# Kernel tuning notes

Measured on AMD Instinct MI355X. Metric: run time of the kernel, lower is better.

The kernel has to match this reference:

```python
import jax, jax.numpy as jnp
import numpy as np

N, K, D = 65536, 1024, 256


def setup_inputs() -> dict:
    key = jax.random.key(0)
    k1, k2 = jax.random.split(key)
    e = jax.random.normal(k1, (N, D), dtype=jnp.float32)
    # module inits codebook uniform in [-1/K, 1/K]
    weight = jax.random.uniform(k2, (K, D), dtype=jnp.float32,
                                minval=-1.0 / K, maxval=1.0 / K)
    return {"e": e, "weight": weight}


def reference(e, weight):
    distances = (jnp.sum(e * e, axis=1, keepdims=True)
                 - 2.0 * jnp.matmul(e, weight.T)
                 + jnp.sum(weight * weight, axis=1))
    encoding_indices = jnp.argmin(distances, axis=1)            # [N]
    # one-hot @ weight is just a gather
    quantized = weight[encoding_indices]                        # [N, D]
    commitment_loss = jnp.mean((jax.lax.stop_gradient(quantized) - e) ** 2)
    counts = jnp.zeros((K,), dtype=jnp.float32).at[encoding_indices].add(1.0)
    codebook_usage = counts.max() / counts.sum()
    # straight-through estimator
    quantized = e + jax.lax.stop_gradient(quantized - e)
    return quantized, encoding_indices, commitment_loss, codebook_usage
```

## Files before the change

### kernel.cpp

```cpp
#include <hip/hip_runtime.h>

typedef __attribute__((ext_vector_type(8))) short short8;
typedef __attribute__((ext_vector_type(4))) float floatx4;

#define N_ROWS 65536
#define K_CB   1024
#define D_DIM  256

#define TAU 4.0e-4f
#define BLINE 520

#define OFF_WN     262144
#define OFF_FIXCNT 266240
#define OFF_HIST   266496
#define OFF_IDX    270592
#define OFF_LIST   532736
#define OFF_PART   794880
#define OFF_WFRAG  827392
#define OFF_KEYS   1351680
#define OFF_WT     1875968

__device__ __forceinline__ float pw128_sq(const float4* p) {
#pragma clang fp contract(off)
    float4 q0 = p[0], q1 = p[1];
    float r0 = q0.x * q0.x, r1 = q0.y * q0.y, r2 = q0.z * q0.z, r3 = q0.w * q0.w;
    float r4 = q1.x * q1.x, r5 = q1.y * q1.y, r6 = q1.z * q1.z, r7 = q1.w * q1.w;
    for (int i = 1; i < 16; ++i) {
        float4 u0 = p[2 * i], u1 = p[2 * i + 1];
        r0 = r0 + u0.x * u0.x; r1 = r1 + u0.y * u0.y;
        r2 = r2 + u0.z * u0.z; r3 = r3 + u0.w * u0.w;
        r4 = r4 + u1.x * u1.x; r5 = r5 + u1.y * u1.y;
        r6 = r6 + u1.z * u1.z; r7 = r7 + u1.w * u1.w;
    }
    return ((r0 + r1) + (r2 + r3)) + ((r4 + r5) + (r6 + r7));
}
__device__ __forceinline__ float pw128_sq_lds(const double* p) {
#pragma clang fp contract(off)
    float r[8];
    #pragma unroll
    for (int j = 0; j < 8; ++j) { float x = (float)p[j]; r[j] = x * x; }
    for (int i = 1; i < 16; ++i) {
        #pragma unroll
        for (int j = 0; j < 8; ++j) { float x = (float)p[8 * i + j]; r[j] = r[j] + x * x; }
    }
    return ((r[0] + r[1]) + (r[2] + r[3])) + ((r[4] + r[5]) + (r[6] + r[7]));
}
__device__ __forceinline__ float rownorm_np(const float* row) {
#pragma clang fp contract(off)
    float s0 = pw128_sq((const float4*)row);
    float s1 = pw128_sq((const float4*)(row + 128));
    return s0 + s1;
}
__device__ __forceinline__ float np_dist(float A, float m, float Ck) {
#pragma clang fp contract(off)
    float Bv = 2.0f * m;
    float t  = A - Bv;
    return t + Ck;
}
__device__ __forceinline__ unsigned short bf16_rne(float x) {
    unsigned u = __float_as_uint(x);
    unsigned r = u + 0x7fff + ((u >> 16) & 1);
    return (unsigned short)(r >> 16);
}

#define PRS 260
__global__ __launch_bounds__(256) void k_prep(
        const float* __restrict__ wg,
        float* __restrict__ wn,
        unsigned short* __restrict__ wfrag, float* __restrict__ wt) {
    __shared__ __align__(16) float es[32 * PRS];
    const int tid = threadIdx.x;
    const int bx  = blockIdx.x;
    if (bx < 4) {
        int row = bx * 256 + tid;
        wn[row] = rownorm_np(wg + (size_t)row * D_DIM);
    } else if (bx < 132) {
        int t = (bx - 4) * 256 + tid;
        int col = t >> 5, kc = t & 31;
        const float4* src = (const float4*)(wg + (size_t)col * D_DIM + kc * 8);
        float4 v0 = src[0], v1 = src[1];
        const float a[8] = {v0.x, v0.y, v0.z, v0.w, v1.x, v1.y, v1.z, v1.w};
        short8 h;
        #pragma unroll
        for (int i = 0; i < 8; ++i) h[i] = (short)bf16_rne(a[i]);
        *(short8*)(wfrag + ((size_t)kc * 1024 + col) * 8) = h;
    } else {
        float (*tw)[PRS] = (float(*)[PRS])es;
        const int cb = bx - 132;
        const int c0 = cb * 32;
        #pragma unroll
        for (int it = 0; it < 8; ++it) {
            int idx = it * 256 + tid;
            int code = idx >> 6, f4 = idx & 63;
            *(float4*)&tw[code][f4 * 4] =
                *(const float4*)(wg + (size_t)(c0 + code) * D_DIM + f4 * 4);
        }
        __syncthreads();
        const int j = tid & 31, dg = tid >> 5;
        #pragma unroll
        for (int dd = 0; dd < 32; ++dd) {
            int d = dd * 8 + dg;
            wt[(size_t)d * K_CB + c0 + j] = tw[j][d];
        }
    }
}

__global__ __launch_bounds__(256, 2) void k_dist(
        const float* __restrict__ eg, const unsigned short* __restrict__ wfrag,
        const float* __restrict__ wn,
        int* __restrict__ idx_ws, int* __restrict__ fixlist, int* __restrict__ fixcnt) {
    __shared__ __align__(16) unsigned short Bs[32 * BLINE];
    __shared__ float wnS[K_CB];
    const int tid  = threadIdx.x;
    const int lane = tid & 63;
    const int wv   = tid >> 6;
    const int q    = lane >> 4;
    const int m15  = lane & 15;
    const int waveRow = blockIdx.x * 128 + wv * 32;

    #pragma unroll
    for (int i = 0; i < 4; ++i) wnS[tid + i * 256] = wn[tid + i * 256];

    short8 afh0[8], afh1[8];
    #pragma unroll
    for (int mt = 0; mt < 2; ++mt) {
        const float* rowp = eg + (size_t)(waveRow + mt * 16 + m15) * D_DIM + q * 8;
        #pragma unroll
        for (int win = 0; win < 8; ++win) {
            const float4* pa = (const float4*)(rowp + win * 32);
            float4 x0 = pa[0], x1 = pa[1];
            const float a[8] = {x0.x, x0.y, x0.z, x0.w, x1.x, x1.y, x1.z, x1.w};
            short8 h;
            #pragma unroll
            for (int i = 0; i < 8; ++i) h[i] = (short)bf16_rne(a[i]);
            if (mt == 0) afh0[win] = h; else afh1[win] = h;
        }
    }

    float best[8], sec[8];
    int bidx[8];
    #pragma unroll
    for (int s = 0; s < 8; ++s) { best[s] = 3.4e38f; sec[s] = 3.4e38f; bidx[s] = 0; }

    for (int cb = 0; cb < 16; ++cb) {
        __syncthreads();
        #pragma unroll
        for (int t = 0; t < 8; ++t) {
            int L = wv * 8 + t;
            const unsigned short* src = wfrag + ((size_t)L * 1024 + cb * 64) * 8 + lane * 8;
            __builtin_amdgcn_global_load_lds(
                (const __attribute__((address_space(1))) unsigned int*)src,
                (__attribute__((address_space(3))) unsigned int*)&Bs[L * BLINE],
                16, 0, 0);
        }
        __syncthreads();

        #pragma unroll
        for (int nt = 0; nt < 4; ++nt) {
            floatx4 acc0 = (floatx4){0.f, 0.f, 0.f, 0.f};
            floatx4 acc1 = (floatx4){0.f, 0.f, 0.f, 0.f};
            #pragma unroll
            for (int win = 0; win < 8; ++win) {
                int kc = win * 4 + q;
                short8 bfh = *(short8*)&Bs[kc * BLINE + (nt * 16 + m15) * 8];
                acc0 = __builtin_amdgcn_mfma_f32_16x16x32_bf16(afh0[win], bfh, acc0, 0, 0, 0);
                acc1 = __builtin_amdgcn_mfma_f32_16x16x32_bf16(afh1[win], bfh, acc1, 0, 0, 0);
            }
            int col = cb * 64 + nt * 16 + m15;
            float Ck = wnS[col];
            #pragma unroll
            for (int reg = 0; reg < 4; ++reg) {
                float d0 = __builtin_fmaf(-2.0f, acc0[reg], Ck);
                bool lt0 = d0 < best[reg];
                sec[reg]  = __builtin_amdgcn_fmed3f(d0, best[reg], sec[reg]);
                best[reg] = fminf(d0, best[reg]);
                bidx[reg] = lt0 ? col : bidx[reg];
                float d1 = __builtin_fmaf(-2.0f, acc1[reg], Ck);
                int s1 = 4 + reg;
                bool lt1 = d1 < best[s1];
                sec[s1]  = __builtin_amdgcn_fmed3f(d1, best[s1], sec[s1]);
                best[s1] = fminf(d1, best[s1]);
                bidx[s1] = lt1 ? col : bidx[s1];
            }
        }
    }

    #pragma unroll
    for (int s = 0; s < 8; ++s) {
        float b = best[s], se = sec[s];
        int ix = bidx[s];
        #pragma unroll
        for (int m = 1; m < 16; m <<= 1) {
            float bo = __shfl_xor(b, m, 64);
            float so = __shfl_xor(se, m, 64);
            int   io = __shfl_xor(ix, m, 64);
            float ns = fminf(fminf(se, so), fmaxf(b, bo));
            if (bo < b || (bo == b && io < ix)) { b = bo; ix = io; }
            se = ns;
        }
        if (m15 == 0) {
            int row = waveRow + (s >> 2) * 16 + q * 4 + (s & 3);
            idx_ws[row] = ix;
            if (se - b < TAU) {
                int p = atomicAdd(fixcnt, 1);
                fixlist[p] = row;
            }
        }
    }
}

#define FG_ROWS 8
__global__ __launch_bounds__(256) void k_fixup(
        const float* __restrict__ eg, const float* __restrict__ wt,
        const float* __restrict__ wnorm,
        const int* __restrict__ fixlist, const int* __restrict__ fixcnt,
        unsigned long long* __restrict__ keys) {
    __shared__ double xs[FG_ROWS][D_DIM];
    __shared__ float AnS[FG_ROWS];
    const int tid = threadIdx.x;
    const int cnt = *fixcnt;
    if (cnt == 0) return;
    const int ngroups = (cnt + FG_ROWS - 1) / FG_ROWS;
    const int ntiles  = ngroups * 2;
    const int rowg = tid >> 7;
    const int cg   = tid & 127;
    for (int t = blockIdx.x; t < ntiles; t += gridDim.x) {
        const int g     = t >> 1;
        const int chunk = t & 1;
        __syncthreads();
        int rows[FG_ROWS];
        #pragma unroll
        for (int i = 0; i < FG_ROWS; ++i) {
            int j = g * FG_ROWS + i;
            rows[i] = fixlist[j < cnt ? j : cnt - 1];
        }
        #pragma unroll
        for (int i = 0; i < FG_ROWS; ++i)
            xs[i][tid] = (double)eg[(size_t)rows[i] * D_DIM + tid];
        __syncthreads();

        if (tid < 16) {
            int row = tid >> 1, half = tid & 1;
            float s = pw128_sq_lds(&xs[row][half * 128]);
            float so = __shfl_xor(s, 1, 64);
            if (half == 0) AnS[row] = s + so;
        }

        const int c0 = chunk * 512 + cg * 4;
        float Cw[4];
        #pragma unroll
        for (int c = 0; c < 4; ++c) Cw[c] = wnorm[c0 + c];

        double s[4][4];
        #pragma unroll
        for (int r = 0; r < 4; ++r)
            #pragma unroll
            for (int c = 0; c < 4; ++c) s[r][c] = 0.0;

        #pragma unroll 2
        for (int d = 0; d < D_DIM; d += 2) {
            float4 wa = *(const float4*)(wt + (size_t)d * K_CB + c0);
            float4 wb = *(const float4*)(wt + (size_t)(d + 1) * K_CB + c0);
            double wad[4] = {(double)wa.x, (double)wa.y, (double)wa.z, (double)wa.w};
            double wbd[4] = {(double)wb.x, (double)wb.y, (double)wb.z, (double)wb.w};
            #pragma unroll
            for (int r = 0; r < 4; ++r) {
                double2 e2 = *(const double2*)&xs[rowg * 4 + r][d];
                #pragma unroll
                for (int c = 0; c < 4; ++c)
                    s[r][c] += e2.x * wad[c] + e2.y * wbd[c];
            }
        }
        __syncthreads();

        #pragma unroll
        for (int r = 0; r < 4; ++r) {
            float An = AnS[rowg * 4 + r];
            unsigned long long key = 0xFFFFFFFFFFFFFFFFull;
            #pragma unroll
            for (int c = 0; c < 4; ++c) {
                float dq = np_dist(An, (float)s[r][c], Cw[c]);
                unsigned u = __float_as_uint(dq);
                unsigned key32 = u ^ (((unsigned)((int)u >> 31)) | 0x80000000u);
                unsigned long long kk =
                    ((unsigned long long)key32 << 32) | (unsigned)(c0 + c);
                key = kk < key ? kk : key;
            }
            #pragma unroll
            for (int m = 1; m < 64; m <<= 1) {
                unsigned long long o = __shfl_xor(key, m, 64);
                key = (o < key) ? o : key;
            }
            int j = g * FG_ROWS + rowg * 4 + r;
            if ((tid & 63) == 0 && j < cnt) atomicMin(&keys[j], key);
        }
    }
}

__global__ void k_fixscatter(const int* __restrict__ fixlist, const int* __restrict__ fixcnt,
                             const unsigned long long* __restrict__ keys,
                             int* __restrict__ idx_ws) {
    const int cnt = *fixcnt;
    for (int j = blockIdx.x * blockDim.x + threadIdx.x; j < cnt;
         j += gridDim.x * blockDim.x)
        idx_ws[fixlist[j]] = (int)(keys[j] & 0xFFFFFFFFull);
}

__global__ void k_final(const float* __restrict__ eg, const float* __restrict__ wg,
                        const int* __restrict__ idx_ws, float* __restrict__ qout,
                        float* __restrict__ iout, int* __restrict__ hist,
                        double* __restrict__ partials) {
    const int tid  = threadIdx.x;
    const int sub  = tid >> 6;
    const int lane = tid & 63;
    const int rowBase = blockIdx.x * 16;
    double acc = 0.0;
    #pragma unroll
    for (int g = 0; g < 4; ++g) {
        int row = rowBase + g * 4 + sub;
        int k = idx_ws[row];
        float4 ev = ((const float4*)(eg + (size_t)row * D_DIM))[lane];
        float4 wv = ((const float4*)(wg + (size_t)k   * D_DIM))[lane];
        float dx = wv.x - ev.x, dy = wv.y - ev.y, dz = wv.z - ev.z, dw = wv.w - ev.w;
        float4 qv = {ev.x + dx, ev.y + dy, ev.z + dz, ev.w + dw};
        ((float4*)(qout + (size_t)row * D_DIM))[lane] = qv;
        acc += (double)(dx * dx) + (double)(dy * dy)
             + (double)(dz * dz) + (double)(dw * dw);
        if (lane == 0) {
            iout[row] = (float)k;
            atomicAdd(&hist[k], 1);
        }
    }
    __shared__ double red[256];
    red[tid] = acc;
    __syncthreads();
    for (int st = 128; st > 0; st >>= 1) {
        if (tid < st) red[tid] += red[tid + st];
        __syncthreads();
    }
    if (tid == 0) partials[blockIdx.x] = red[0];
}

__global__ void k_scalars(const int* __restrict__ hist, const double* __restrict__ partials,
                          float* __restrict__ sout) {
    const int tid = threadIdx.x;
    double s = 0.0;
    for (int j = tid; j < N_ROWS / 16; j += 256) s += partials[j];
    int m = 0;
    for (int j = tid; j < K_CB; j += 256) m = max(m, hist[j]);
    __shared__ double rs[256];
    __shared__ int    rm[256];
    rs[tid] = s; rm[tid] = m;
    __syncthreads();
    for (int st = 128; st > 0; st >>= 1) {
        if (tid < st) { rs[tid] += rs[tid + st]; rm[tid] = max(rm[tid], rm[tid + st]); }
        __syncthreads();
    }
    if (tid == 0) {
        sout[0] = (float)(rs[0] / (double)((size_t)N_ROWS * D_DIM));
        sout[1] = (float)rm[0] / 65536.0f;
    }
}

extern "C" void kernel_launch(void* const* d_in, const int* in_sizes, int n_in,
                              void* d_out, int out_size, void* d_ws, size_t ws_size,
                              hipStream_t stream) {
    const float* e = (const float*)d_in[0];
    const float* w = (const float*)d_in[1];
    float* out  = (float*)d_out;
    float* qout = out;
    float* iout = out + (size_t)N_ROWS * D_DIM;
    float* sout = iout + N_ROWS;

    char* ws = (char*)d_ws;
    float*  wn       = (float*) (ws + OFF_WN);
    int*    fixcnt   = (int*)   (ws + OFF_FIXCNT);
    int*    hist     = (int*)   (ws + OFF_HIST);
    int*    idxp     = (int*)   (ws + OFF_IDX);
    int*    list     = (int*)   (ws + OFF_LIST);
    double* partials = (double*)(ws + OFF_PART);
    unsigned short* wfrag = (unsigned short*)(ws + OFF_WFRAG);
    unsigned long long* keys = (unsigned long long*)(ws + OFF_KEYS);
    float*  wt       = (float*) (ws + OFF_WT);

    hipMemsetAsync(ws + OFF_FIXCNT, 0, 4352, stream);
    hipMemsetAsync(ws + OFF_KEYS, 0xFF, 524288, stream);

    hipLaunchKernelGGL(k_prep,       dim3(164),         dim3(256), 0, stream, w, wn, wfrag, wt);
    hipLaunchKernelGGL(k_dist,       dim3(512),         dim3(256), 0, stream, e, wfrag, wn, idxp, list, fixcnt);
    hipLaunchKernelGGL(k_fixup,      dim3(2048),        dim3(256), 0, stream, e, wt, wn, list, fixcnt, keys);
    hipLaunchKernelGGL(k_fixscatter, dim3(64),          dim3(256), 0, stream, list, fixcnt, keys, idxp);
    hipLaunchKernelGGL(k_final,      dim3(N_ROWS / 16), dim3(256), 0, stream, e, w, idxp, qout, iout, hist, partials);
    hipLaunchKernelGGL(k_scalars,    dim3(1),           dim3(256), 0, stream, hist, partials, sout);
}
```

Before: 314.7 us.

## Double-buffer codebook tiles in k_dist and use fp32 top-2 rescoring in fixup

```diff
diff --git a/kernel.cpp b/kernel.cpp
--- a/kernel.cpp
+++ b/kernel.cpp
@@ -34,17 +34,6 @@
     }
     return ((r0 + r1) + (r2 + r3)) + ((r4 + r5) + (r6 + r7));
 }
-__device__ __forceinline__ float pw128_sq_lds(const double* p) {
-#pragma clang fp contract(off)
-    float r[8];
-    #pragma unroll
-    for (int j = 0; j < 8; ++j) { float x = (float)p[j]; r[j] = x * x; }
-    for (int i = 1; i < 16; ++i) {
-        #pragma unroll
-        for (int j = 0; j < 8; ++j) { float x = (float)p[8 * i + j]; r[j] = r[j] + x * x; }
-    }
-    return ((r[0] + r[1]) + (r[2] + r[3])) + ((r[4] + r[5]) + (r[6] + r[7]));
-}
 __device__ __forceinline__ float rownorm_np(const float* row) {
 #pragma clang fp contract(off)
     float s0 = pw128_sq((const float4*)row);
@@ -61,6 +50,11 @@
     unsigned u = __float_as_uint(x);
     unsigned r = u + 0x7fff + ((u >> 16) & 1);
     return (unsigned short)(r >> 16);
+}
+__device__ __forceinline__ unsigned long long dist_key(float d, int idx) {
+    unsigned u = __float_as_uint(d);
+    unsigned k32 = u ^ (((unsigned)((int)u >> 31)) | 0x80000000u);
+    return ((unsigned long long)k32 << 32) | (unsigned)idx;
 }
 
 #define PRS 260
@@ -109,7 +103,7 @@
         const float* __restrict__ eg, const unsigned short* __restrict__ wfrag,
         const float* __restrict__ wn,
         int* __restrict__ idx_ws, int* __restrict__ fixlist, int* __restrict__ fixcnt) {
-    __shared__ __align__(16) unsigned short Bs[32 * BLINE];
+    __shared__ __align__(16) unsigned short Bs[2][32 * BLINE];
     __shared__ float wnS[K_CB];
     const int tid  = threadIdx.x;
     const int lane = tid & 63;
@@ -142,19 +136,31 @@
     #pragma unroll
     for (int s = 0; s < 8; ++s) { best[s] = 3.4e38f; sec[s] = 3.4e38f; bidx[s] = 0; }
 
+    #pragma unroll
+    for (int t = 0; t < 8; ++t) {
+        int L = wv * 8 + t;
+        const unsigned short* src = wfrag + ((size_t)L * 1024) * 8 + lane * 8;
+        __builtin_amdgcn_global_load_lds(
+            (const __attribute__((address_space(1))) unsigned int*)src,
+            (__attribute__((address_space(3))) unsigned int*)&Bs[0][L * BLINE],
+            16, 0, 0);
+    }
+    __syncthreads();
+
     for (int cb = 0; cb < 16; ++cb) {
-        __syncthreads();
-        #pragma unroll
-        for (int t = 0; t < 8; ++t) {
-            int L = wv * 8 + t;
-            const unsigned short* src = wfrag + ((size_t)L * 1024 + cb * 64) * 8 + lane * 8;
-            __builtin_amdgcn_global_load_lds(
-                (const __attribute__((address_space(1))) unsigned int*)src,
-                (__attribute__((address_space(3))) unsigned int*)&Bs[L * BLINE],
-                16, 0, 0);
-        }
-        __syncthreads();
-
+        const int p = cb & 1;
+        if (cb < 15) {
+            #pragma unroll
+            for (int t = 0; t < 8; ++t) {
+                int L = wv * 8 + t;
+                const unsigned short* src =
+                    wfrag + ((size_t)L * 1024 + (cb + 1) * 64) * 8 + lane * 8;
+                __builtin_amdgcn_global_load_lds(
+                    (const __attribute__((address_space(1))) unsigned int*)src,
+                    (__attribute__((address_space(3))) unsigned int*)&Bs[p ^ 1][L * BLINE],
+                    16, 0, 0);
+            }
+        }
         #pragma unroll
         for (int nt = 0; nt < 4; ++nt) {
             floatx4 acc0 = (floatx4){0.f, 0.f, 0.f, 0.f};
@@ -162,7 +168,7 @@
             #pragma unroll
             for (int win = 0; win < 8; ++win) {
                 int kc = win * 4 + q;
-                short8 bfh = *(short8*)&Bs[kc * BLINE + (nt * 16 + m15) * 8];
+                short8 bfh = *(short8*)&Bs[p][kc * BLINE + (nt * 16 + m15) * 8];
                 acc0 = __builtin_amdgcn_mfma_f32_16x16x32_bf16(afh0[win], bfh, acc0, 0, 0, 0);
                 acc1 = __builtin_amdgcn_mfma_f32_16x16x32_bf16(afh1[win], bfh, acc1, 0, 0, 0);
             }
@@ -183,6 +189,7 @@
                 bidx[s1] = lt1 ? col : bidx[s1];
             }
         }
+        __syncthreads();
     }
 
     #pragma unroll
@@ -211,13 +218,14 @@
 
 #define FG_ROWS 8
 __global__ __launch_bounds__(256) void k_fixup(
-        const float* __restrict__ eg, const float* __restrict__ wt,
-        const float* __restrict__ wnorm,
+        const float* __restrict__ eg, const float* __restrict__ wg,
+        const float* __restrict__ wt, const float* __restrict__ wnorm,
         const int* __restrict__ fixlist, const int* __restrict__ fixcnt,
         unsigned long long* __restrict__ keys) {
-    __shared__ double xs[FG_ROWS][D_DIM];
+    __shared__ __align__(16) float xs[FG_ROWS][D_DIM];
     __shared__ float AnS[FG_ROWS];
-    const int tid = threadIdx.x;
+    const int tid  = threadIdx.x;
+    const int lane = tid & 63;
     const int cnt = *fixcnt;
     if (cnt == 0) return;
     const int ngroups = (cnt + FG_ROWS - 1) / FG_ROWS;
@@ -236,14 +244,14 @@
         }
         #pragma unroll
         for (int i = 0; i < FG_ROWS; ++i)
-            xs[i][tid] = (double)eg[(size_t)rows[i] * D_DIM + tid];
+            xs[i][tid] = eg[(size_t)rows[i] * D_DIM + tid];
         __syncthreads();
 
         if (tid < 16) {
             int row = tid >> 1, half = tid & 1;
-            float s = pw128_sq_lds(&xs[row][half * 128]);
-            float so = __shfl_xor(s, 1, 64);
-            if (half == 0) AnS[row] = s + so;
+            float sN = pw128_sq((const float4*)&xs[row][half * 128]);
+            float so = __shfl_xor(sN, 1, 64);
+            if (half == 0) AnS[row] = sN + so;
         }
 
         const int c0 = chunk * 512 + cg * 4;
@@ -251,48 +259,67 @@
         #pragma unroll
         for (int c = 0; c < 4; ++c) Cw[c] = wnorm[c0 + c];
 
-        double s[4][4];
+        float s[4][4];
         #pragma unroll
         for (int r = 0; r < 4; ++r)
             #pragma unroll
-            for (int c = 0; c < 4; ++c) s[r][c] = 0.0;
+            for (int c = 0; c < 4; ++c) s[r][c] = 0.f;
 
         #pragma unroll 2
         for (int d = 0; d < D_DIM; d += 2) {
             float4 wa = *(const float4*)(wt + (size_t)d * K_CB + c0);
             float4 wb = *(const float4*)(wt + (size_t)(d + 1) * K_CB + c0);
-            double wad[4] = {(double)wa.x, (double)wa.y, (double)wa.z, (double)wa.w};
-            double wbd[4] = {(double)wb.x, (double)wb.y, (double)wb.z, (double)wb.w};
             #pragma unroll
             for (int r = 0; r < 4; ++r) {
-                double2 e2 = *(const double2*)&xs[rowg * 4 + r][d];
-                #pragma unroll
-                for (int c = 0; c < 4; ++c)
-                    s[r][c] += e2.x * wad[c] + e2.y * wbd[c];
+                float2 e2 = *(const float2*)&xs[rowg * 4 + r][d];
+                s[r][0] += e2.x * wa.x + e2.y * wb.x;
+                s[r][1] += e2.x * wa.y + e2.y * wb.y;
+                s[r][2] += e2.x * wa.z + e2.y * wb.z;
+                s[r][3] += e2.x * wa.w + e2.y * wb.w;
             }
         }
         __syncthreads();
 
         #pragma unroll
         for (int r = 0; r < 4; ++r) {
-            float An = AnS[rowg * 4 + r];
-            unsigned long long key = 0xFFFFFFFFFFFFFFFFull;
+            const int R = rowg * 4 + r;
+            float An = AnS[R];
+            unsigned long long kb = 0xFFFFFFFFFFFFFFFFull, ks = 0xFFFFFFFFFFFFFFFFull;
             #pragma unroll
             for (int c = 0; c < 4; ++c) {
-                float dq = np_dist(An, (float)s[r][c], Cw[c]);
-                unsigned u = __float_as_uint(dq);
-                unsigned key32 = u ^ (((unsigned)((int)u >> 31)) | 0x80000000u);
-                unsigned long long kk =
-                    ((unsigned long long)key32 << 32) | (unsigned)(c0 + c);
-                key = kk < key ? kk : key;
+                float dq = np_dist(An, s[r][c], Cw[c]);
+                unsigned long long kk = dist_key(dq, c0 + c);
+                if (kk < kb) { ks = kb; kb = kk; }
+                else if (kk < ks) { ks = kk; }
             }
             #pragma unroll
             for (int m = 1; m < 64; m <<= 1) {
-                unsigned long long o = __shfl_xor(key, m, 64);
-                key = (o < key) ? o : key;
-            }
-            int j = g * FG_ROWS + rowg * 4 + r;
-            if ((tid & 63) == 0 && j < cnt) atomicMin(&keys[j], key);
+                unsigned long long ko = __shfl_xor(kb, m, 64);
+                unsigned long long so = __shfl_xor(ks, m, 64);
+                if (ko < kb) { ks = (so < kb) ? so : kb; kb = ko; }
+                else         { ks = (ko < ks) ? ko : ks; }
+            }
+            int cand = (int)((lane < 32 ? kb : ks) & 0xFFFFFFFFull);
+            const float* wrow = wg + (size_t)cand * D_DIM + (lane & 31) * 8;
+            const float* erow = &xs[R][(lane & 31) * 8];
+            double sm = 0.0;
+            #pragma unroll
+            for (int jj = 0; jj < 8; ++jj)
+                sm += (double)erow[jj] * (double)wrow[jj];
+            #pragma unroll
+            for (int m = 1; m < 32; m <<= 1) sm += __shfl_xor(sm, m, 64);
+            double smo = __shfl_xor(sm, 32, 64);
+            if (lane == 0) {
+                int i0 = (int)(kb & 0xFFFFFFFFull);
+                int i1 = (int)(ks & 0xFFFFFFFFull);
+                float d0 = np_dist(An, (float)sm,  wnorm[i0]);
+                float d1 = np_dist(An, (float)smo, wnorm[i1]);
+                unsigned long long k0 = dist_key(d0, i0);
+                unsigned long long k1 = dist_key(d1, i1);
+                unsigned long long kf = k0 < k1 ? k0 : k1;
+                int j = g * FG_ROWS + R;
+                if (j < cnt) atomicMin(&keys[j], kf);
+            }
         }
     }
 }
@@ -388,7 +415,7 @@
 
     hipLaunchKernelGGL(k_prep,       dim3(164),         dim3(256), 0, stream, w, wn, wfrag, wt);
     hipLaunchKernelGGL(k_dist,       dim3(512),         dim3(256), 0, stream, e, wfrag, wn, idxp, list, fixcnt);
-    hipLaunchKernelGGL(k_fixup,      dim3(2048),        dim3(256), 0, stream, e, wt, wn, list, fixcnt, keys);
+    hipLaunchKernelGGL(k_fixup,      dim3(2048),        dim3(256), 0, stream, e, w, wt, wn, list, fixcnt, keys);
     hipLaunchKernelGGL(k_fixscatter, dim3(64),          dim3(256), 0, stream, list, fixcnt, keys, idxp);
     hipLaunchKernelGGL(k_final,      dim3(N_ROWS / 16), dim3(256), 0, stream, e, w, idxp, qout, iout, hist, partials);
     hipLaunchKernelGGL(k_scalars,    dim3(1),           dim3(256), 0, stream, hist, partials, sout);
```

New measurement: 296.9 us. 1.06x faster.
